# Optimization experiments

Hardware: AMD Instinct MI355X
Metric: run time of the kernel (lower is better)

## Reference

```python
import jax, jax.numpy as jnp
import numpy as np

N = 50000   # nodes
E = 400000  # edges per metapath
M = 3       # metapaths
L = 2       # HAN layers
IN = 256    # input feat = hidden*heads so layers stack
H = 4       # heads
DO = 64     # out per head
D = H * DO  # 256


def setup_inputs() -> dict:
    key = jax.random.key(0)
    ks = jax.random.split(key, 12)
    x = jax.random.normal(ks[0], (M, N, IN), jnp.float32)
    src = jax.random.randint(ks[1], (M, E), 0, N, jnp.int32)
    dst = jax.random.randint(ks[2], (M, E), 0, N, jnp.int32)
    W_gat = jax.random.normal(ks[3], (L, M, IN, D), jnp.float32) * 0.06
    attn_l = jax.random.normal(ks[4], (L, M, H, DO), jnp.float32) * 0.1
    attn_r = jax.random.normal(ks[5], (L, M, H, DO), jnp.float32) * 0.1
    bias_gat = jnp.zeros((L, M, D), jnp.float32)
    W1 = jax.random.normal(ks[6], (D, DO), jnp.float32) * 0.06
    b1 = jnp.zeros((DO,), jnp.float32)
    W2 = jax.random.normal(ks[7], (DO, 1), jnp.float32) * 0.1
    Wp = jax.random.normal(ks[8], (D, DO), jnp.float32) * 0.06
    bp = jnp.zeros((DO,), jnp.float32)
    return {"x": x, "W_gat": W_gat, "attn_l": attn_l, "attn_r": attn_r,
            "bias_gat": bias_gat, "W1": W1, "b1": b1, "W2": W2,
            "Wp": Wp, "bp": bp, "src": src, "dst": dst}


def gat_conv(h, src, dst, W, al, ar, bias):
    # h: (N, IN) -> feat: (N, H, DO)
    feat = (h @ W).reshape(N, H, DO)
    el = jnp.einsum('nhd,hd->nh', feat, al)   # (N, H)
    er = jnp.einsum('nhd,hd->nh', feat, ar)   # (N, H)
    e = jax.nn.leaky_relu(el[src] + er[dst], 0.2)  # (E, H)
    # numerically stable edge softmax over incoming edges per dst node
    mx = jax.ops.segment_max(e, dst, num_segments=N)  # (N, H)
    mx = jnp.where(jnp.isfinite(mx), mx, 0.0)         # empty segments
    ex = jnp.exp(e - mx[dst])                         # (E, H)
    denom = jax.ops.segment_sum(ex, dst, num_segments=N)  # (N, H)
    msg = jax.ops.segment_sum(ex[:, :, None] * feat[src], dst, num_segments=N)  # (N,H,DO)
    out = msg / jnp.maximum(denom, 1e-9)[:, :, None]
    out = out + bias.reshape(H, DO)
    return jax.nn.elu(out).reshape(N, D)  # flatten(1)


def reference(x, W_gat, attn_l, attn_r, bias_gat, W1, b1, W2, Wp, bp, src, dst):
    h = [x[i] for i in range(M)]
    for l in range(L):
        h = [gat_conv(h[i], src[i], dst[i], W_gat[l, i], attn_l[l, i],
                      attn_r[l, i], bias_gat[l, i]) for i in range(M)]
    z = jnp.stack(h, axis=1)  # (N, M, D)
    # semantic attention: small MLP -> per-metapath scalar, softmax over M
    w = (jnp.tanh(z @ W1 + b1) @ W2).mean(0)   # (M, 1)
    beta = jax.nn.softmax(w, axis=0)           # (M, 1)
    agg = (z * beta[None]).sum(1)              # (N, D)
    return agg @ Wp + bp                       # (N, DO)
```

## Files before the change

kernel.cpp:

```cpp
#include <hip/hip_runtime.h>

#define NN 50000
#define EE 400000
#define MM 3
#define CHUNK 2048
#define NCHUNK ((NN + CHUNK - 1) / CHUNK)

typedef float f32x4 __attribute__((ext_vector_type(4)));
typedef short s16x8 __attribute__((ext_vector_type(8)));
typedef _Float16 half_t;
typedef _Float16 h16x2 __attribute__((ext_vector_type(2)));
typedef _Float16 h16x4 __attribute__((ext_vector_type(4)));

union FU { float f; unsigned u; };

__device__ inline short bfhi(float x) {
    FU c; c.f = x;
    unsigned u = c.u;
    return (short)((u + 0x7fffu + ((u >> 16) & 1u)) >> 16);
}
__device__ inline float bf2f(short h) {
    FU c; c.u = ((unsigned)(unsigned short)h) << 16;
    return c.f;
}
__device__ inline float h2f(short bits) {
    union HU { short s; _Float16 h; } u; u.s = bits; return (float)u.h;
}


__global__ __launch_bounds__(256) void init_kernel(int* counts, float* wsum) {
    int idx = blockIdx.x * 256 + threadIdx.x;
    if (idx < MM * NN) counts[idx] = 0;
    if (idx < MM) wsum[idx] = 0.0f;
}

__global__ __launch_bounds__(256) void hist_kernel(const int* __restrict__ dst,
                                                   int* __restrict__ counts) {
    int m = blockIdx.y;
    int e = blockIdx.x * 256 + threadIdx.x;
    if (e < EE) atomicAdd(&counts[m * NN + dst[m * EE + e]], 1);
}

__global__ __launch_bounds__(256) void scan_partial_kernel(const int* __restrict__ counts,
                                                           int* __restrict__ rp,
                                                           int* __restrict__ bsum) {
    int m = blockIdx.y, ch = blockIdx.x;
    const int* c = counts + m * NN;
    int* r = rp + m * (NN + 1);
    int t = threadIdx.x, lane = t & 63, wave = t >> 6;
    int i0 = ch * CHUNK + t * 8;
    int v[8]; int s = 0;
#pragma unroll
    for (int k = 0; k < 8; ++k) { int i = i0 + k; v[k] = (i < NN) ? c[i] : 0; s += v[k]; }
    int incl = s;
#pragma unroll
    for (int off = 1; off < 64; off <<= 1) {
        int u = __shfl_up(incl, off);
        if (lane >= off) incl += u;
    }
    int excl = incl - s;
    __shared__ int wsh[4];
    if (lane == 63) wsh[wave] = incl;
    __syncthreads();
    int woff = 0;
    for (int w = 0; w < wave; ++w) woff += wsh[w];
    int run = excl + woff;
#pragma unroll
    for (int k = 0; k < 8; ++k) { int i = i0 + k; if (i < NN) r[i] = run; run += v[k]; }
    if (t == 255) bsum[m * NCHUNK + ch] = woff + incl;
}

__global__ __launch_bounds__(256) void scan_top_kernel(int* __restrict__ bsum) {
    int wave = threadIdx.x >> 6, lane = threadIdx.x & 63;
    if (wave < MM) {
        int v = (lane < NCHUNK) ? bsum[wave * NCHUNK + lane] : 0;
        int incl = v;
#pragma unroll
        for (int off = 1; off < 64; off <<= 1) {
            int u = __shfl_up(incl, off);
            if (lane >= off) incl += u;
        }
        if (lane < NCHUNK) bsum[wave * NCHUNK + lane] = incl - v;
    }
}

__global__ __launch_bounds__(256) void scan_add_kernel(const int* __restrict__ bsum,
                                                       int* __restrict__ rp,
                                                       int* __restrict__ cur) {
    int m = blockIdx.y, ch = blockIdx.x;
    int off = bsum[m * NCHUNK + ch];
    int* r = rp + m * (NN + 1);
    int* q = cur + m * (NN + 1);
    int i0 = ch * CHUNK + threadIdx.x * 8;
#pragma unroll
    for (int k = 0; k < 8; ++k) {
        int i = i0 + k;
        if (i < NN) { int val = r[i] + off; r[i] = val; q[i] = val; }
    }
    if (ch == 0 && threadIdx.x == 0) r[NN] = EE;
}

__global__ __launch_bounds__(256) void scatter_kernel(const int* __restrict__ src,
                                                      const int* __restrict__ dst,
                                                      int* __restrict__ cursor,
                                                      int* __restrict__ ssrc) {
    int m = blockIdx.y;
    int e = blockIdx.x * 256 + threadIdx.x;
    if (e < EE) {
        int d = dst[m * EE + e];
        int pos = atomicAdd(&cursor[m * (NN + 1) + d], 1);
        __builtin_nontemporal_store(src[m * EE + e], &ssrc[m * EE + pos]);
    }
}


#define WG_ELEMS (6 * 256 * 256)
#define W_TOT (WG_ELEMS + 128 * 256)

__global__ __launch_bounds__(256) void splitW_kernel(const float* __restrict__ Wg,
                                                     const float* __restrict__ W1,
                                                     const float* __restrict__ Wp,
                                                     short* __restrict__ Whi,
                                                     short* __restrict__ Wlo) {
    int idx = blockIdx.x * 256 + threadIdx.x;
    if (idx >= W_TOT) return;
    float v;
    if (idx < WG_ELEMS) {
        int mat = idx >> 16, rem = idx & 65535;
        int n = rem >> 8, k = rem & 255;
        v = Wg[mat * 65536 + k * 256 + n];
    } else {
        int i2 = idx - WG_ELEMS;
        int n = i2 >> 8, k = i2 & 255;
        v = (n < 64) ? W1[k * 64 + n] : Wp[k * 64 + n - 64];
    }
    short h = bfhi(v);
    Whi[idx] = h;
    Wlo[idx] = bfhi(v - bf2f(h));
}


template<int AMODE>
__global__ __launch_bounds__(256) void mfma_gemm(
    const float* __restrict__ Af, const half_t* __restrict__ A16,
    const short* __restrict__ Wthi, const short* __restrict__ Wtlo,
    half_t* __restrict__ featA,
    const float* __restrict__ alA, const float* __restrict__ arA,
    float* __restrict__ elA, float* __restrict__ erA) {
    __shared__ short Ah[64 * 32], Al[64 * 32], Bh[256 * 32], Bl[256 * 32];
    const int m = blockIdx.y;
    const int t = threadIdx.x;
    const int lane = t & 63;
    const int wn = t >> 6;
    const int row0 = blockIdx.x * 64;
    const float*  A0 = Af + (size_t)m * NN * 256;
    const short*  A1 = (const short*)(A16 + (size_t)m * NN * 256);
    const short*  Bgh = Wthi + (size_t)m * 65536;
    const short*  Bgl = Wtlo + (size_t)m * 65536;
    half_t* Ch = featA + (size_t)m * NN * 256;
    const float* al = alA + m * 256;
    const float* ar = arA + m * 256;
    float* el = elA + (size_t)m * NN * 4;
    float* er = erA + (size_t)m * NN * 4;
    f32x4 acc[4][4] = {};

    const int r = t >> 2, c0 = t & 3;
    const int aoff = r * 32 + ((c0 ^ ((r >> 1) & 3)) << 3);
    const int arow = row0 + r;
    const bool aval = (arow < NN);

    s16x8 praw = {0,0,0,0,0,0,0,0};
    float4 pf0 = make_float4(0.f,0.f,0.f,0.f), pf1 = make_float4(0.f,0.f,0.f,0.f);

    if (AMODE == 1) {
        if (aval) praw = *(const s16x8*)(A1 + (size_t)arow * 256 + c0 * 8);
    } else {
        if (aval) {
            pf0 = *(const float4*)(A0 + (size_t)arow * 256 + c0 * 8);
            pf1 = *(const float4*)(A0 + (size_t)arow * 256 + c0 * 8 + 4);
        }
    }

    for (int k0 = 0; k0 < 256; k0 += 32) {
        {
            float v[8];
            if (AMODE == 1) {
#pragma unroll
                for (int j = 0; j < 8; ++j) v[j] = h2f(praw[j]);
            } else {
                v[0] = pf0.x; v[1] = pf0.y; v[2] = pf0.z; v[3] = pf0.w;
                v[4] = pf1.x; v[5] = pf1.y; v[6] = pf1.z; v[7] = pf1.w;
            }
            s16x8 hh, ll;
#pragma unroll
            for (int j = 0; j < 8; ++j) {
                short hs = bfhi(v[j]);
                hh[j] = hs;
                ll[j] = bfhi(v[j] - bf2f(hs));
            }
            *(s16x8*)&Ah[aoff] = hh;
            *(s16x8*)&Al[aoff] = ll;
        }
#pragma unroll
        for (int u = 0; u < 4; ++u) {
            int n = u * 64 + (t >> 2), c = t & 3;
            s16x8 h = *(const s16x8*)(Bgh + (size_t)n * 256 + k0 + c * 8);
            s16x8 l = *(const s16x8*)(Bgl + (size_t)n * 256 + k0 + c * 8);
            int off = n * 32 + ((c ^ ((n >> 1) & 3)) << 3);
            *(s16x8*)&Bh[off] = h;
            *(s16x8*)&Bl[off] = l;
        }
        __syncthreads();
        if (k0 + 32 < 256) {
            if (AMODE == 1) {
                praw = s16x8{0,0,0,0,0,0,0,0};
                if (aval) praw = *(const s16x8*)(A1 + (size_t)arow * 256 + k0 + 32 + c0 * 8);
            } else {
                pf0 = make_float4(0.f,0.f,0.f,0.f); pf1 = make_float4(0.f,0.f,0.f,0.f);
                if (aval) {
                    pf0 = *(const float4*)(A0 + (size_t)arow * 256 + k0 + 32 + c0 * 8);
                    pf1 = *(const float4*)(A0 + (size_t)arow * 256 + k0 + 32 + c0 * 8 + 4);
                }
            }
        }
        int fr = lane & 15, ac = lane >> 4;
        s16x8 afh[4], afl[4], bfh[4], bfl[4];
#pragma unroll
        for (int i = 0; i < 4; ++i) {
            int rr = i * 16 + fr;
            int off = rr * 32 + ((ac ^ ((rr >> 1) & 3)) << 3);
            afh[i] = *(const s16x8*)&Ah[off];
            afl[i] = *(const s16x8*)&Al[off];
        }
#pragma unroll
        for (int j = 0; j < 4; ++j) {
            int n = wn * 64 + j * 16 + fr;
            int off = n * 32 + ((ac ^ ((n >> 1) & 3)) << 3);
            bfh[j] = *(const s16x8*)&Bh[off];
            bfl[j] = *(const s16x8*)&Bl[off];
        }
#pragma unroll
        for (int i = 0; i < 4; ++i)
#pragma unroll
            for (int j = 0; j < 4; ++j) {
                acc[i][j] = __builtin_amdgcn_mfma_f32_16x16x32_bf16(afh[i], bfh[j], acc[i][j], 0, 0, 0);
                acc[i][j] = __builtin_amdgcn_mfma_f32_16x16x32_bf16(afh[i], bfl[j], acc[i][j], 0, 0, 0);
                acc[i][j] = __builtin_amdgcn_mfma_f32_16x16x32_bf16(afl[i], bfh[j], acc[i][j], 0, 0, 0);
            }
        __syncthreads();
    }

#pragma unroll
    for (int i = 0; i < 4; ++i) {
        int rbase = row0 + i * 16 + (lane >> 4) * 4;
#pragma unroll
        for (int j = 0; j < 4; ++j) {
            int col = wn * 64 + j * 16 + (lane & 15);
#pragma unroll
            for (int q = 0; q < 4; ++q) {
                int row = rbase + q;
                if (row < NN) Ch[(size_t)row * 256 + col] = (half_t)acc[i][j][q];
            }
        }
    }
    float alv[4], arv[4];
#pragma unroll
    for (int j = 0; j < 4; ++j) {
        int col = wn * 64 + j * 16 + (lane & 15);
        alv[j] = al[col];
        arv[j] = ar[col];
    }
#pragma unroll
    for (int i = 0; i < 4; ++i)
#pragma unroll
        for (int q = 0; q < 4; ++q) {
            float ep = acc[i][0][q] * alv[0] + acc[i][1][q] * alv[1]
                     + acc[i][2][q] * alv[2] + acc[i][3][q] * alv[3];
            float rp_ = acc[i][0][q] * arv[0] + acc[i][1][q] * arv[1]
                      + acc[i][2][q] * arv[2] + acc[i][3][q] * arv[3];
#pragma unroll
            for (int msk = 1; msk < 16; msk <<= 1) {
                ep += __shfl_xor(ep, msk);
                rp_ += __shfl_xor(rp_, msk);
            }
            if ((lane & 15) == 0) {
                int row = row0 + i * 16 + (lane >> 4) * 4 + q;
                if (row < NN) {
                    el[row * 4 + wn] = ep;
                    er[row * 4 + wn] = rp_;
                }
            }
        }
}


__global__ __launch_bounds__(256) void sem_gemm(
    const half_t* __restrict__ A16,
    const short* __restrict__ Wthi, const short* __restrict__ Wtlo,
    float* __restrict__ P,
    const float* __restrict__ b1, const float* __restrict__ w2,
    float* __restrict__ wsum,
    int nrows) {
    __shared__ short Ah[128 * 32], Al[128 * 32], Bh[128 * 32], Bl[128 * 32];
    const int t = threadIdx.x;
    const int lane = t & 63;
    const int wave = t >> 6;
    const int wm = wave >> 1, wn = wave & 1;
    const int row0 = blockIdx.x * 128;
    const short* A1 = (const short*)A16;
    f32x4 acc[4][4] = {};

    const int r0 = (t * 2) >> 2, c0 = (t * 2) & 3;
    const int r1 = (t * 2 + 1) >> 2, c1 = (t * 2 + 1) & 3;
    const int aoff0 = r0 * 32 + ((c0 ^ ((r0 >> 1) & 3)) << 3);
    const int aoff1 = r1 * 32 + ((c1 ^ ((r1 >> 1) & 3)) << 3);
    const int arow0 = row0 + r0, arow1 = row0 + r1;

    s16x8 p0 = {0,0,0,0,0,0,0,0}, p1 = {0,0,0,0,0,0,0,0};
    if (arow0 < nrows) p0 = *(const s16x8*)(A1 + (size_t)arow0 * 256 + c0 * 8);
    if (arow1 < nrows) p1 = *(const s16x8*)(A1 + (size_t)arow1 * 256 + c1 * 8);

    for (int k0 = 0; k0 < 256; k0 += 32) {
        {
            s16x8 hh, ll;
#pragma unroll
            for (int j = 0; j < 8; ++j) {
                float v = h2f(p0[j]);
                short hs = bfhi(v);
                hh[j] = hs; ll[j] = bfhi(v - bf2f(hs));
            }
            *(s16x8*)&Ah[aoff0] = hh; *(s16x8*)&Al[aoff0] = ll;
#pragma unroll
            for (int j = 0; j < 8; ++j) {
                float v = h2f(p1[j]);
                short hs = bfhi(v);
                hh[j] = hs; ll[j] = bfhi(v - bf2f(hs));
            }
            *(s16x8*)&Ah[aoff1] = hh; *(s16x8*)&Al[aoff1] = ll;
        }
#pragma unroll
        for (int u = 0; u < 2; ++u) {
            int idx = t * 2 + u;
            int n = idx >> 2, c = idx & 3;
            s16x8 h = *(const s16x8*)(Wthi + (size_t)n * 256 + k0 + c * 8);
            s16x8 l = *(const s16x8*)(Wtlo + (size_t)n * 256 + k0 + c * 8);
            int off = n * 32 + ((c ^ ((n >> 1) & 3)) << 3);
            *(s16x8*)&Bh[off] = h;
            *(s16x8*)&Bl[off] = l;
        }
        __syncthreads();
        if (k0 + 32 < 256) {
            p0 = s16x8{0,0,0,0,0,0,0,0}; p1 = s16x8{0,0,0,0,0,0,0,0};
            if (arow0 < nrows) p0 = *(const s16x8*)(A1 + (size_t)arow0 * 256 + k0 + 32 + c0 * 8);
            if (arow1 < nrows) p1 = *(const s16x8*)(A1 + (size_t)arow1 * 256 + k0 + 32 + c1 * 8);
        }
        int fr = lane & 15, ac = lane >> 4;
        s16x8 afh[4], afl[4], bfh[4], bfl[4];
#pragma unroll
        for (int i = 0; i < 4; ++i) {
            int rr = wm * 64 + i * 16 + fr;
            int off = rr * 32 + ((ac ^ ((rr >> 1) & 3)) << 3);
            afh[i] = *(const s16x8*)&Ah[off];
            afl[i] = *(const s16x8*)&Al[off];
        }
#pragma unroll
        for (int j = 0; j < 4; ++j) {
            int n = wn * 64 + j * 16 + fr;
            int off = n * 32 + ((ac ^ ((n >> 1) & 3)) << 3);
            bfh[j] = *(const s16x8*)&Bh[off];
            bfl[j] = *(const s16x8*)&Bl[off];
        }
#pragma unroll
        for (int i = 0; i < 4; ++i)
#pragma unroll
            for (int j = 0; j < 4; ++j) {
                acc[i][j] = __builtin_amdgcn_mfma_f32_16x16x32_bf16(afh[i], bfh[j], acc[i][j], 0, 0, 0);
                acc[i][j] = __builtin_amdgcn_mfma_f32_16x16x32_bf16(afh[i], bfl[j], acc[i][j], 0, 0, 0);
                acc[i][j] = __builtin_amdgcn_mfma_f32_16x16x32_bf16(afl[i], bfh[j], acc[i][j], 0, 0, 0);
            }
        __syncthreads();
    }

    float* wp = (float*)&Ah[0];
    if (t < 3) wp[t] = 0.f;
    __syncthreads();
    int fr = lane & 15, ac = lane >> 4;
    if (wn == 0) {
        float b1v[4], w2v[4];
#pragma unroll
        for (int j = 0; j < 4; ++j) {
            int col = j * 16 + fr;
            b1v[j] = b1[col];
            w2v[j] = w2[col];
        }
#pragma unroll
        for (int i = 0; i < 4; ++i)
#pragma unroll
            for (int q = 0; q < 4; ++q) {
                float ep = tanhf(acc[i][0][q] + b1v[0]) * w2v[0]
                         + tanhf(acc[i][1][q] + b1v[1]) * w2v[1]
                         + tanhf(acc[i][2][q] + b1v[2]) * w2v[2]
                         + tanhf(acc[i][3][q] + b1v[3]) * w2v[3];
#pragma unroll
                for (int msk = 1; msk < 16; msk <<= 1) ep += __shfl_xor(ep, msk);
                if (fr == 0) {
                    int row = row0 + wm * 64 + i * 16 + ac * 4 + q;
                    if (row < nrows) atomicAdd(&wp[row / NN], ep);
                }
            }
    } else {
#pragma unroll
        for (int i = 0; i < 4; ++i) {
            int rbase = row0 + wm * 64 + i * 16 + ac * 4;
#pragma unroll
            for (int j = 0; j < 4; ++j) {
                int pcol = j * 16 + fr;
#pragma unroll
                for (int q = 0; q < 4; ++q) {
                    int row = rbase + q;
                    if (row < nrows) P[(size_t)row * 64 + pcol] = acc[i][j][q];
                }
            }
        }
    }
    __syncthreads();
    if (t < 3) atomicAdd(&wsum[t], wp[t]);
}


__global__ __launch_bounds__(256) void agg_edges_kernel(const half_t* __restrict__ featA,
                                                        const float* __restrict__ elA,
                                                        const float* __restrict__ erA,
                                                        const int* __restrict__ row_ptrA,
                                                        const int* __restrict__ ssrcA,
                                                        const float* __restrict__ biasL,
                                                        half_t* __restrict__ HbA) {
    const int m = blockIdx.y;
    const half_t* feat = featA + (size_t)m * NN * 256;
    const float* el = elA + (size_t)m * NN * 4;
    const float* er = erA + (size_t)m * NN * 4;
    const int* row_ptr = row_ptrA + (size_t)m * (NN + 1);
    const int* ssrc = ssrcA + (size_t)m * EE;
    const float* bias = biasL + m * 256;
    half_t* out = HbA + (size_t)m * NN * 256;

    int wave = threadIdx.x >> 6;
    int lane = threadIdx.x & 63;
    int n = blockIdx.x * 4 + wave;
    int h = lane >> 4;
    int beg = row_ptr[n], end = row_ptr[n + 1];
    float ern = er[n * 4 + h];
    const h16x4* fb = (const h16x4*)feat + lane;
    float a0A = 0.f, a1A = 0.f, a2A = 0.f, a3A = 0.f, dA = 0.f;
    float a0B = 0.f, a1B = 0.f, a2B = 0.f, a3B = 0.f, dB = 0.f;
    int j = beg;
    for (; j + 1 < end; j += 2) {
        int sA = ssrc[j], sB = ssrc[j + 1];
        float eA = el[sA * 4 + h];
        float eB = el[sB * 4 + h];
        h16x4 fA = fb[(size_t)sA * 64];
        h16x4 fB = fb[(size_t)sB * 64];
        eA += ern; eA = eA > 0.f ? eA : 0.2f * eA; float wA = __expf(eA);
        eB += ern; eB = eB > 0.f ? eB : 0.2f * eB; float wB = __expf(eB);
        a0A = fmaf(wA, (float)fA.x, a0A); a1A = fmaf(wA, (float)fA.y, a1A);
        a2A = fmaf(wA, (float)fA.z, a2A); a3A = fmaf(wA, (float)fA.w, a3A); dA += wA;
        a0B = fmaf(wB, (float)fB.x, a0B); a1B = fmaf(wB, (float)fB.y, a1B);
        a2B = fmaf(wB, (float)fB.z, a2B); a3B = fmaf(wB, (float)fB.w, a3B); dB += wB;
    }
    if (j < end) {
        int s = ssrc[j];
        float e = el[s * 4 + h] + ern;
        e = e > 0.f ? e : 0.2f * e;
        float wgt = __expf(e);
        h16x4 f = fb[(size_t)s * 64];
        a0A = fmaf(wgt, (float)f.x, a0A); a1A = fmaf(wgt, (float)f.y, a1A);
        a2A = fmaf(wgt, (float)f.z, a2A); a3A = fmaf(wgt, (float)f.w, a3A); dA += wgt;
    }
    float den = fmaxf(dA + dB, 1e-9f);
    int col = lane * 4;
    float o0 = (a0A + a0B) / den + bias[col + 0];
    float o1 = (a1A + a1B) / den + bias[col + 1];
    float o2 = (a2A + a2B) / den + bias[col + 2];
    float o3 = (a3A + a3B) / den + bias[col + 3];
    o0 = o0 > 0.f ? o0 : __expf(o0) - 1.0f;
    o1 = o1 > 0.f ? o1 : __expf(o1) - 1.0f;
    o2 = o2 > 0.f ? o2 : __expf(o2) - 1.0f;
    o3 = o3 > 0.f ? o3 : __expf(o3) - 1.0f;
    h16x4 ov; ov.x = (half_t)o0; ov.y = (half_t)o1; ov.z = (half_t)o2; ov.w = (half_t)o3;
    ((h16x4*)(out + (size_t)n * 256))[lane] = ov;
}


__global__ void beta_kernel(const float* __restrict__ wsum, float* __restrict__ beta) {
    if (threadIdx.x == 0 && blockIdx.x == 0) {
        float w0 = wsum[0] / (float)NN, w1 = wsum[1] / (float)NN, w2 = wsum[2] / (float)NN;
        float mx = fmaxf(w0, fmaxf(w1, w2));
        float e0 = __expf(w0 - mx), e1 = __expf(w1 - mx), e2 = __expf(w2 - mx);
        float s = e0 + e1 + e2;
        beta[0] = e0 / s; beta[1] = e1 / s; beta[2] = e2 / s;
    }
}

__global__ __launch_bounds__(256) void combine_out_kernel(const float* __restrict__ P,
                                                          const float* __restrict__ beta,
                                                          const float* __restrict__ bp,
                                                          float* __restrict__ out) {
    int idx4 = blockIdx.x * 256 + threadIdx.x;
    if (idx4 >= NN * 64 / 4) return;
    float b0 = beta[0], b1 = beta[1], b2 = beta[2];
    float4 p0 = ((const float4*)P)[idx4];
    float4 p1 = ((const float4*)P)[idx4 + NN * 16];
    float4 p2 = ((const float4*)P)[idx4 + NN * 32];
    float4 bpv = *(const float4*)(bp + ((idx4 * 4) & 63));
    float4 o;
    o.x = b0 * p0.x + b1 * p1.x + b2 * p2.x + bpv.x;
    o.y = b0 * p0.y + b1 * p1.y + b2 * p2.y + bpv.y;
    o.z = b0 * p0.z + b1 * p1.z + b2 * p2.z + bpv.z;
    o.w = b0 * p0.w + b1 * p1.w + b2 * p2.w + bpv.w;
    ((float4*)out)[idx4] = o;
}


extern "C" void kernel_launch(void* const* d_in, const int* in_sizes, int n_in,
                              void* d_out, int out_size, void* d_ws, size_t ws_size,
                              hipStream_t stream) {
    const float* x        = (const float*)d_in[0];
    const float* W_gat    = (const float*)d_in[1];
    const float* attn_l   = (const float*)d_in[2];
    const float* attn_r   = (const float*)d_in[3];
    const float* bias_gat = (const float*)d_in[4];
    const float* W1       = (const float*)d_in[5];
    const float* b1       = (const float*)d_in[6];
    const float* W2       = (const float*)d_in[7];
    const float* Wp       = (const float*)d_in[8];
    const float* bp       = (const float*)d_in[9];
    const int*   src      = (const int*)d_in[10];
    const int*   dst      = (const int*)d_in[11];
    float* out = (float*)d_out;

    char* ws = (char*)d_ws;
    size_t off = 0;
    auto alloc = [&](size_t bytes) { size_t o = off; off = (off + bytes + 255) & ~(size_t)255; return o; };
    half_t* Hb      = (half_t*)(ws + alloc((size_t)MM * NN * 256 * 2));
    half_t* feat    = (half_t*)(ws + alloc((size_t)MM * NN * 256 * 2));
    float*  P       = (float*)(ws + alloc((size_t)MM * NN * 64 * 4));
    float*  el      = (float*)(ws + alloc((size_t)MM * NN * 4 * 4));
    float*  er      = (float*)(ws + alloc((size_t)MM * NN * 4 * 4));
    int*    counts  = (int*)(ws + alloc((size_t)MM * NN * 4));
    int*    row_ptr = (int*)(ws + alloc((size_t)MM * (NN + 1) * 4));
    int*    cursor  = (int*)(ws + alloc((size_t)MM * (NN + 1) * 4));
    int*    ssrc    = (int*)(ws + alloc((size_t)MM * EE * 4));
    int*    bsum    = (int*)(ws + alloc((size_t)MM * NCHUNK * 4));
    short*  Whi     = (short*)(ws + alloc((size_t)W_TOT * 2));
    short*  Wlo     = (short*)(ws + alloc((size_t)W_TOT * 2));
    float*  wsum    = (float*)(ws + alloc(16));
    float*  beta    = (float*)(ws + alloc(16));

    init_kernel<<<dim3((MM * NN + 255) / 256), 256, 0, stream>>>(counts, wsum);
    hist_kernel<<<dim3((EE + 255) / 256, MM), 256, 0, stream>>>(dst, counts);
    scan_partial_kernel<<<dim3(NCHUNK, MM), 256, 0, stream>>>(counts, row_ptr, bsum);
    scan_top_kernel<<<dim3(1), 256, 0, stream>>>(bsum);
    scan_add_kernel<<<dim3(NCHUNK, MM), 256, 0, stream>>>(bsum, row_ptr, cursor);
    scatter_kernel<<<dim3((EE + 255) / 256, MM), 256, 0, stream>>>(src, dst, cursor, ssrc);
    splitW_kernel<<<dim3((W_TOT + 255) / 256), 256, 0, stream>>>(W_gat, W1, Wp, Whi, Wlo);

    const int rowTiles = (NN + 63) / 64;

    for (int l = 0; l < 2; ++l) {
        const short* wh = Whi + (size_t)l * MM * 65536;
        const short* wl = Wlo + (size_t)l * MM * 65536;
        const float* alp = attn_l + (size_t)l * MM * 256;
        const float* arp = attn_r + (size_t)l * MM * 256;
        if (l == 0)
            mfma_gemm<0><<<dim3(rowTiles, MM), 256, 0, stream>>>(
                x, nullptr, wh, wl, feat, alp, arp, el, er);
        else
            mfma_gemm<1><<<dim3(rowTiles, MM), 256, 0, stream>>>(
                nullptr, Hb, wh, wl, feat, alp, arp, el, er);
        agg_edges_kernel<<<dim3(NN / 4, MM), 256, 0, stream>>>(
            feat, el, er, row_ptr, ssrc, bias_gat + (size_t)l * MM * 256, Hb);
    }

    sem_gemm<<<dim3((MM * NN + 127) / 128), 256, 0, stream>>>(
        Hb, Whi + WG_ELEMS, Wlo + WG_ELEMS, P, b1, W2, wsum, MM * NN);
    beta_kernel<<<dim3(1), 64, 0, stream>>>(wsum, beta);
    combine_out_kernel<<<dim3((NN * 16 + 255) / 256), 256, 0, stream>>>(P, beta, bp, out);
}
```

Baseline: 666.9 us.

## Precompute per-edge attention weights in separate kernel and unroll aggregation by four

```diff
diff --git a/kernel.cpp b/kernel.cpp
--- a/kernel.cpp
+++ b/kernel.cpp
@@ -9,7 +9,6 @@
 typedef float f32x4 __attribute__((ext_vector_type(4)));
 typedef short s16x8 __attribute__((ext_vector_type(8)));
 typedef _Float16 half_t;
-typedef _Float16 h16x2 __attribute__((ext_vector_type(2)));
 typedef _Float16 h16x4 __attribute__((ext_vector_type(4)));
 
 union FU { float f; unsigned u; };
@@ -103,13 +102,14 @@
 __global__ __launch_bounds__(256) void scatter_kernel(const int* __restrict__ src,
                                                       const int* __restrict__ dst,
                                                       int* __restrict__ cursor,
-                                                      int* __restrict__ ssrc) {
+                                                      long long* __restrict__ spair) {
     int m = blockIdx.y;
     int e = blockIdx.x * 256 + threadIdx.x;
     if (e < EE) {
         int d = dst[m * EE + e];
         int pos = atomicAdd(&cursor[m * (NN + 1) + d], 1);
-        __builtin_nontemporal_store(src[m * EE + e], &ssrc[m * EE + pos]);
+        long long p = ((long long)d << 32) | (unsigned)src[m * EE + e];
+        __builtin_nontemporal_store(p, &spair[(size_t)m * EE + pos]);
     }
 }
 
@@ -428,19 +428,40 @@
 }
 
 
+__global__ __launch_bounds__(256) void edge_w_kernel(const long long* __restrict__ spairA,
+                                                     const float* __restrict__ elA,
+                                                     const float* __restrict__ erA,
+                                                     float* __restrict__ wTA) {
+    const int m = blockIdx.y;
+    int j = blockIdx.x * 256 + threadIdx.x;
+    if (j >= EE) return;
+    long long p = spairA[(size_t)m * EE + j];
+    int s = (int)(unsigned)(p & 0xffffffffLL);
+    int d = (int)(p >> 32);
+    const float4 e_l = ((const float4*)(elA + (size_t)m * NN * 4))[s];
+    const float4 e_r = ((const float4*)(erA + (size_t)m * NN * 4))[d];
+    float* wT = wTA + (size_t)m * 4 * EE;
+    float e0 = e_l.x + e_r.x; e0 = e0 > 0.f ? e0 : 0.2f * e0;
+    float e1 = e_l.y + e_r.y; e1 = e1 > 0.f ? e1 : 0.2f * e1;
+    float e2 = e_l.z + e_r.z; e2 = e2 > 0.f ? e2 : 0.2f * e2;
+    float e3 = e_l.w + e_r.w; e3 = e3 > 0.f ? e3 : 0.2f * e3;
+    wT[0 * EE + j] = __expf(e0);
+    wT[1 * EE + j] = __expf(e1);
+    wT[2 * EE + j] = __expf(e2);
+    wT[3 * EE + j] = __expf(e3);
+}
+
+
 __global__ __launch_bounds__(256) void agg_edges_kernel(const half_t* __restrict__ featA,
-                                                        const float* __restrict__ elA,
-                                                        const float* __restrict__ erA,
+                                                        const float* __restrict__ wTA,
+                                                        const long long* __restrict__ spairA,
                                                         const int* __restrict__ row_ptrA,
-                                                        const int* __restrict__ ssrcA,
                                                         const float* __restrict__ biasL,
                                                         half_t* __restrict__ HbA) {
     const int m = blockIdx.y;
     const half_t* feat = featA + (size_t)m * NN * 256;
-    const float* el = elA + (size_t)m * NN * 4;
-    const float* er = erA + (size_t)m * NN * 4;
     const int* row_ptr = row_ptrA + (size_t)m * (NN + 1);
-    const int* ssrc = ssrcA + (size_t)m * EE;
+    const long long* spair = spairA + (size_t)m * EE;
     const float* bias = biasL + m * 256;
     half_t* out = HbA + (size_t)m * NN * 256;
 
@@ -448,40 +469,46 @@
     int lane = threadIdx.x & 63;
     int n = blockIdx.x * 4 + wave;
     int h = lane >> 4;
+    const float* wh = wTA + (size_t)m * 4 * EE + (size_t)h * EE;
     int beg = row_ptr[n], end = row_ptr[n + 1];
-    float ern = er[n * 4 + h];
     const h16x4* fb = (const h16x4*)feat + lane;
     float a0A = 0.f, a1A = 0.f, a2A = 0.f, a3A = 0.f, dA = 0.f;
     float a0B = 0.f, a1B = 0.f, a2B = 0.f, a3B = 0.f, dB = 0.f;
+    float a0C = 0.f, a1C = 0.f, a2C = 0.f, a3C = 0.f, dC = 0.f;
+    float a0D = 0.f, a1D = 0.f, a2D = 0.f, a3D = 0.f, dD = 0.f;
     int j = beg;
-    for (; j + 1 < end; j += 2) {
-        int sA = ssrc[j], sB = ssrc[j + 1];
-        float eA = el[sA * 4 + h];
-        float eB = el[sB * 4 + h];
+    for (; j + 3 < end; j += 4) {
+        int sA = (int)(unsigned)spair[j];
+        int sB = (int)(unsigned)spair[j + 1];
+        int sC = (int)(unsigned)spair[j + 2];
+        int sD = (int)(unsigned)spair[j + 3];
+        float wA = wh[j], wB = wh[j + 1], wC = wh[j + 2], wD = wh[j + 3];
         h16x4 fA = fb[(size_t)sA * 64];
         h16x4 fB = fb[(size_t)sB * 64];
-        eA += ern; eA = eA > 0.f ? eA : 0.2f * eA; float wA = __expf(eA);
-        eB += ern; eB = eB > 0.f ? eB : 0.2f * eB; float wB = __expf(eB);
+        h16x4 fC = fb[(size_t)sC * 64];
+        h16x4 fD = fb[(size_t)sD * 64];
         a0A = fmaf(wA, (float)fA.x, a0A); a1A = fmaf(wA, (float)fA.y, a1A);
         a2A = fmaf(wA, (float)fA.z, a2A); a3A = fmaf(wA, (float)fA.w, a3A); dA += wA;
         a0B = fmaf(wB, (float)fB.x, a0B); a1B = fmaf(wB, (float)fB.y, a1B);
         a2B = fmaf(wB, (float)fB.z, a2B); a3B = fmaf(wB, (float)fB.w, a3B); dB += wB;
-    }
-    if (j < end) {
-        int s = ssrc[j];
-        float e = el[s * 4 + h] + ern;
-        e = e > 0.f ? e : 0.2f * e;
-        float wgt = __expf(e);
+        a0C = fmaf(wC, (float)fC.x, a0C); a1C = fmaf(wC, (float)fC.y, a1C);
+        a2C = fmaf(wC, (float)fC.z, a2C); a3C = fmaf(wC, (float)fC.w, a3C); dC += wC;
+        a0D = fmaf(wD, (float)fD.x, a0D); a1D = fmaf(wD, (float)fD.y, a1D);
+        a2D = fmaf(wD, (float)fD.z, a2D); a3D = fmaf(wD, (float)fD.w, a3D); dD += wD;
+    }
+    for (; j < end; ++j) {
+        int s = (int)(unsigned)spair[j];
+        float w = wh[j];
         h16x4 f = fb[(size_t)s * 64];
-        a0A = fmaf(wgt, (float)f.x, a0A); a1A = fmaf(wgt, (float)f.y, a1A);
-        a2A = fmaf(wgt, (float)f.z, a2A); a3A = fmaf(wgt, (float)f.w, a3A); dA += wgt;
-    }
-    float den = fmaxf(dA + dB, 1e-9f);
+        a0A = fmaf(w, (float)f.x, a0A); a1A = fmaf(w, (float)f.y, a1A);
+        a2A = fmaf(w, (float)f.z, a2A); a3A = fmaf(w, (float)f.w, a3A); dA += w;
+    }
+    float den = fmaxf((dA + dB) + (dC + dD), 1e-9f);
     int col = lane * 4;
-    float o0 = (a0A + a0B) / den + bias[col + 0];
-    float o1 = (a1A + a1B) / den + bias[col + 1];
-    float o2 = (a2A + a2B) / den + bias[col + 2];
-    float o3 = (a3A + a3B) / den + bias[col + 3];
+    float o0 = ((a0A + a0B) + (a0C + a0D)) / den + bias[col + 0];
+    float o1 = ((a1A + a1B) + (a1C + a1D)) / den + bias[col + 1];
+    float o2 = ((a2A + a2B) + (a2C + a2D)) / den + bias[col + 2];
+    float o3 = ((a3A + a3B) + (a3C + a3D)) / den + bias[col + 3];
     o0 = o0 > 0.f ? o0 : __expf(o0) - 1.0f;
     o1 = o1 > 0.f ? o1 : __expf(o1) - 1.0f;
     o2 = o2 > 0.f ? o2 : __expf(o2) - 1.0f;
@@ -549,7 +576,8 @@
     int*    counts  = (int*)(ws + alloc((size_t)MM * NN * 4));
     int*    row_ptr = (int*)(ws + alloc((size_t)MM * (NN + 1) * 4));
     int*    cursor  = (int*)(ws + alloc((size_t)MM * (NN + 1) * 4));
-    int*    ssrc    = (int*)(ws + alloc((size_t)MM * EE * 4));
+    long long* spair = (long long*)(ws + alloc((size_t)MM * EE * 8));
+    float*  wT      = (float*)(ws + alloc((size_t)MM * 4 * EE * 4));
     int*    bsum    = (int*)(ws + alloc((size_t)MM * NCHUNK * 4));
     short*  Whi     = (short*)(ws + alloc((size_t)W_TOT * 2));
     short*  Wlo     = (short*)(ws + alloc((size_t)W_TOT * 2));
@@ -561,7 +589,7 @@
     scan_partial_kernel<<<dim3(NCHUNK, MM), 256, 0, stream>>>(counts, row_ptr, bsum);
     scan_top_kernel<<<dim3(1), 256, 0, stream>>>(bsum);
     scan_add_kernel<<<dim3(NCHUNK, MM), 256, 0, stream>>>(bsum, row_ptr, cursor);
-    scatter_kernel<<<dim3((EE + 255) / 256, MM), 256, 0, stream>>>(src, dst, cursor, ssrc);
+    scatter_kernel<<<dim3((EE + 255) / 256, MM), 256, 0, stream>>>(src, dst, cursor, spair);
     splitW_kernel<<<dim3((W_TOT + 255) / 256), 256, 0, stream>>>(W_gat, W1, Wp, Whi, Wlo);
 
     const int rowTiles = (NN + 63) / 64;
@@ -577,8 +605,9 @@
         else
             mfma_gemm<1><<<dim3(rowTiles, MM), 256, 0, stream>>>(
                 nullptr, Hb, wh, wl, feat, alp, arp, el, er);
+        edge_w_kernel<<<dim3((EE + 255) / 256, MM), 256, 0, stream>>>(spair, el, er, wT);
         agg_edges_kernel<<<dim3(NN / 4, MM), 256, 0, stream>>>(
-            feat, el, er, row_ptr, ssrc, bias_gat + (size_t)l * MM * 256, Hb);
+            feat, wT, spair, row_ptr, bias_gat + (size_t)l * MM * 256, Hb);
     }
 
     sem_gemm<<<dim3((MM * NN + 127) / 128), 256, 0, stream>>>(
```

Result: slower. 682.7 us (+2.4%).
